# Optimization experiments

Measured on AMD Instinct MI355X. Metric: run time of the kernel, lower is better.

## Reference

```python
import jax, jax.numpy as jnp
import numpy as np

B, S = 128, 1024
IN_NUM, IN_STATE = 64, 16
FEAT = 256
HID = 512
NUM_CLS = 32
EMB_WORD, EMB_DIM = 32, 4
LN_EPS = 1e-5


def _layer_norm(x):
    mu = jnp.mean(x, axis=-1, keepdims=True)
    var = jnp.var(x, axis=-1, keepdims=True)
    return (x - mu) * jax.lax.rsqrt(var + LN_EPS)


def setup_inputs() -> dict:
    key = jax.random.key(0)
    ks = jax.random.split(key, 20)
    w = lambda k, shape: jax.random.normal(k, shape, dtype=jnp.float32) * 0.05
    inp = {
        'x_num': jax.random.normal(ks[0], (B, S, IN_NUM), dtype=jnp.float32),
        'x_state': jax.random.randint(ks[1], (B, S, IN_STATE), 0, EMB_WORD),
        # numeric-branch MLP (2 layers)
        'num_w0': w(ks[2], (FEAT, IN_NUM)), 'num_b0': jnp.zeros((FEAT,), jnp.float32),
        'num_w1': w(ks[3], (FEAT, FEAT)),   'num_b1': jnp.zeros((FEAT,), jnp.float32),
        # state-branch embedding + MLP
        'emb': w(ks[4], (EMB_WORD, EMB_DIM)),
        'st_w0': w(ks[5], (FEAT, IN_STATE * EMB_DIM)), 'st_b0': jnp.zeros((FEAT,), jnp.float32),
        'st_w1': w(ks[6], (FEAT, FEAT)),               'st_b1': jnp.zeros((FEAT,), jnp.float32),
        # LSTM gate weights: input dim = 2*FEAT
        'Wii': w(ks[7], (HID, 2 * FEAT)),  'Whi': w(ks[8], (HID, HID)),
        'Wif': w(ks[9], (HID, 2 * FEAT)),  'Whf': w(ks[10], (HID, HID)),
        'Wig': w(ks[11], (HID, 2 * FEAT)), 'Whg': w(ks[12], (HID, HID)),
        'Wio': w(ks[13], (HID, 2 * FEAT)), 'Who': w(ks[14], (HID, HID)),
        'Bii': jnp.zeros((HID,), jnp.float32), 'Bhi': jnp.zeros((HID,), jnp.float32),
        'Bif': jnp.zeros((HID,), jnp.float32), 'Bhf': jnp.zeros((HID,), jnp.float32),
        'Big': jnp.zeros((HID,), jnp.float32), 'Bhg': jnp.zeros((HID,), jnp.float32),
        'Bio': jnp.zeros((HID,), jnp.float32), 'Bho': jnp.zeros((HID,), jnp.float32),
        'out_w': w(ks[15], (NUM_CLS, HID)), 'out_b': jnp.zeros((NUM_CLS,), jnp.float32),
    }
    return inp


def _forward(x_num, x_state, num_w0, num_b0, num_w1, num_b1, emb,
             st_w0, st_b0, st_w1, st_b1,
             Wii, Whi, Wif, Whf, Wig, Whg, Wio, Who,
             Bii, Bhi, Bif, Bhf, Big, Bhg, Bio, Bho,
             out_w, out_b):
    b, s = x_num.shape[0], x_num.shape[1]
    # numeric branch: Linear -> relu -> LayerNorm (dropout is identity in eval)
    h = _layer_norm(jax.nn.relu(x_num @ num_w0.T + num_b0))
    h = _layer_norm(jax.nn.relu(h @ num_w1.T + num_b1))
    # state branch: embedding lookup, flatten per step, then MLP
    e = emb[x_state].reshape(b, s, -1)                      # [B,S,IN_STATE*EMB_DIM]
    g = _layer_norm(jax.nn.relu(e @ st_w0.T + st_b0))
    g = _layer_norm(jax.nn.relu(g @ st_w1.T + st_b1))
    x = jnp.concatenate([h, g], axis=2)                     # [B,S,2*FEAT]

    hid = Whi.shape[0]
    h0 = jnp.zeros((b, hid), x.dtype)
    c0 = jnp.zeros((b, hid), x.dtype)

    def step(carry, x_t):
        h_t, c_t = carry
        i_t = jax.nn.sigmoid(x_t @ Wii.T + h_t @ Whi.T + Bii + Bhi)
        f_t = jax.nn.sigmoid(x_t @ Wif.T + h_t @ Whf.T + Bif + Bhf)
        g_t = jnp.tanh(x_t @ Wig.T + h_t @ Whg.T + Big + Bhg)
        o_t = jax.nn.sigmoid(x_t @ Wio.T + h_t @ Who.T + Bio + Bho)
        c_new = f_t * c_t + i_t * g_t
        h_new = o_t * jnp.tanh(c_new)
        return (h_new, c_new), None

    (h_last, _), _ = jax.lax.scan(step, (h0, c0), jnp.swapaxes(x, 0, 1))
    return h_last @ out_w.T + out_b                          # [B, num_cls]


def reference(x_num, x_state, num_w0, num_b0, num_w1, num_b1, emb,
              st_w0, st_b0, st_w1, st_b1,
              Wii, Whi, Wif, Whf, Wig, Whg, Wio, Who,
              Bii, Bhi, Bif, Bhf, Big, Bhg, Bio, Bho,
              out_w, out_b):
    return _forward(x_num, x_state, num_w0, num_b0, num_w1, num_b1, emb,
                    st_w0, st_b0, st_w1, st_b1,
                    Wii, Whi, Wif, Whf, Wig, Whg, Wio, Who,
                    Bii, Bhi, Bif, Bhf, Big, Bhg, Bio, Bho,
                    out_w, out_b)
```

## Files before the change

### kernel.cpp

```cpp
#include <hip/hip_runtime.h>
#include <hip/hip_bf16.h>

typedef __attribute__((ext_vector_type(4))) float f4;
typedef __attribute__((ext_vector_type(4))) float f32x4;
typedef __attribute__((ext_vector_type(8))) short bf16x8;
typedef __attribute__((ext_vector_type(4))) unsigned u32x4;
typedef unsigned long long ull;

#define OFF_XCAT   0ull
#define OFF_WCAT   134217728ull
#define OFF_BIAS   138412032ull
#define OFF_HW     138420224ull
#define OFF_CTR    138944512ull
#define WS_NEED    138945536ull

__device__ inline unsigned short f2bf(float x){
  unsigned u = __float_as_uint(x);
  unsigned r = (u + 0x7FFFu + ((u >> 16) & 1u)) >> 16;
  return (unsigned short)r;
}
__device__ inline float bf2f(unsigned short s){ return __uint_as_float(((unsigned)s) << 16); }

__global__ void __launch_bounds__(256) diag_write(float* out, float val){
  out[blockIdx.x * 256 + threadIdx.x] = val;
}

__global__ void __launch_bounds__(256) prep_w(
    const float* Wii, const float* Wif, const float* Wig, const float* Wio,
    const float* Whi, const float* Whf, const float* Whg, const float* Who,
    const float* Bii, const float* Bif, const float* Big, const float* Bio,
    const float* Bhi, const float* Bhf, const float* Bhg, const float* Bho,
    unsigned short* Wcat, float* bias_cat){
  int e = blockIdx.x * 256 + threadIdx.x;
  int col = e >> 10, k = e & 1023;
  int u = col >> 2, g = col & 3;
  float v;
  if (k < 512){
    const float* p = (g==0)?Wii:((g==1)?Wif:((g==2)?Wig:Wio));
    v = p[u*512 + k];
  } else {
    const float* p = (g==0)?Whi:((g==1)?Whf:((g==2)?Whg:Who));
    v = p[u*512 + (k-512)];
  }
  Wcat[e] = f2bf(v);
  if (e < 2048){
    int u2 = e >> 2, g2 = e & 3;
    const float* bx = (g2==0)?Bii:((g2==1)?Bif:((g2==2)?Big:Bio));
    const float* bh = (g2==0)?Bhi:((g2==1)?Bhf:((g2==2)?Bhg:Bho));
    bias_cat[e] = bx[u2] + bh[u2];
  }
}

__global__ void __launch_bounds__(256) stageA_fused(
    const float* __restrict__ xnum, const int* __restrict__ xstate,
    const float* __restrict__ emb,
    const float* __restrict__ num_w0, const float* __restrict__ num_b0,
    const float* __restrict__ num_w1, const float* __restrict__ num_b1,
    const float* __restrict__ st_w0,  const float* __restrict__ st_b0,
    const float* __restrict__ st_w1,  const float* __restrict__ st_b1,
    unsigned short* __restrict__ Xcat){
  __shared__ float Wt[32*256];
  __shared__ float xb[16*68];
  __shared__ float h1[16*260];
  int tid = threadIdx.x;
  long tok0 = (long)blockIdx.x * 16;
  int tg = tid >> 6, c4 = tid & 63;

  #pragma unroll 1
  for (int br = 0; br < 2; ++br){
    const float* W0 = br ? st_w0 : num_w0;
    const float* b0 = br ? st_b0 : num_b0;
    const float* W1 = br ? st_w1 : num_w1;
    const float* b1 = br ? st_b1 : num_b1;

    __syncthreads();
    if (br == 0){
      int tk = tid >> 4, q = tid & 15;
      f4 v = *(const f4*)(xnum + (tok0+tk)*64 + q*4);
      float* d = xb + tk*68 + q*4;
      d[0]=v.x; d[1]=v.y; d[2]=v.z; d[3]=v.w;
    } else {
      int tk = tid >> 4, j = tid & 15;
      int idx = xstate[(tok0+tk)*16 + j];
      f4 v = *(const f4*)(emb + idx*4);
      float* d = xb + tk*68 + j*4;
      d[0]=v.x; d[1]=v.y; d[2]=v.z; d[3]=v.w;
    }

    float acc[4][4];
    { f4 bv = *(const f4*)(b0 + c4*4);
      #pragma unroll
      for (int j=0;j<4;j++){ acc[j][0]=bv.x; acc[j][1]=bv.y; acc[j][2]=bv.z; acc[j][3]=bv.w; } }
    for (int kh=0; kh<2; ++kh){
      __syncthreads();
      { int c = tid;
        const f4* src = (const f4*)(W0 + c*64 + kh*32);
        #pragma unroll
        for (int q=0;q<8;q++){
          f4 v = src[q];
          Wt[(q*4+0)*256 + c] = v.x; Wt[(q*4+1)*256 + c] = v.y;
          Wt[(q*4+2)*256 + c] = v.z; Wt[(q*4+3)*256 + c] = v.w;
        }
      }
      __syncthreads();
      for (int kq=0; kq<8; kq++){
        int k0 = kh*32 + kq*4;
        f4 a0 = *(const f4*)(xb + (tg*4+0)*68 + k0);
        f4 a1 = *(const f4*)(xb + (tg*4+1)*68 + k0);
        f4 a2 = *(const f4*)(xb + (tg*4+2)*68 + k0);
        f4 a3 = *(const f4*)(xb + (tg*4+3)*68 + k0);
        f4 w0 = *(const f4*)(Wt + (kq*4+0)*256 + c4*4);
        f4 w1 = *(const f4*)(Wt + (kq*4+1)*256 + c4*4);
        f4 w2 = *(const f4*)(Wt + (kq*4+2)*256 + c4*4);
        f4 w3 = *(const f4*)(Wt + (kq*4+3)*256 + c4*4);
        #pragma unroll
        for (int j=0;j<4;j++){
          f4 a = (j==0)?a0:((j==1)?a1:((j==2)?a2:a3));
          #pragma unroll
          for (int d=0; d<4; d++)
            acc[j][d] += a.x*w0[d] + a.y*w1[d] + a.z*w2[d] + a.w*w3[d];
        }
      }
    }
    #pragma unroll
    for (int j=0;j<4;j++){
      float v0=fmaxf(acc[j][0],0.f), v1=fmaxf(acc[j][1],0.f);
      float v2=fmaxf(acc[j][2],0.f), v3=fmaxf(acc[j][3],0.f);
      float s1 = v0+v1+v2+v3, s2 = v0*v0+v1*v1+v2*v2+v3*v3;
      for (int off=1; off<64; off<<=1){ s1 += __shfl_xor(s1, off); s2 += __shfl_xor(s2, off); }
      float mu = s1 * (1.f/256.f);
      float rs = rsqrtf(s2*(1.f/256.f) - mu*mu + 1e-5f);
      f4 o; o.x=(v0-mu)*rs; o.y=(v1-mu)*rs; o.z=(v2-mu)*rs; o.w=(v3-mu)*rs;
      *(f4*)(h1 + (tg*4+j)*260 + c4*4) = o;
    }

    float ac2[4][4];
    { f4 bv = *(const f4*)(b1 + c4*4);
      #pragma unroll
      for (int j=0;j<4;j++){ ac2[j][0]=bv.x; ac2[j][1]=bv.y; ac2[j][2]=bv.z; ac2[j][3]=bv.w; } }
    for (int kh=0; kh<8; ++kh){
      __syncthreads();
      { int c = tid;
        const f4* src = (const f4*)(W1 + c*256 + kh*32);
        #pragma unroll
        for (int q=0;q<8;q++){
          f4 v = src[q];
          Wt[(q*4+0)*256 + c] = v.x; Wt[(q*4+1)*256 + c] = v.y;
          Wt[(q*4+2)*256 + c] = v.z; Wt[(q*4+3)*256 + c] = v.w;
        }
      }
      __syncthreads();
      for (int kq=0; kq<8; kq++){
        int k0 = kh*32 + kq*4;
        f4 a0 = *(const f4*)(h1 + (tg*4+0)*260 + k0);
        f4 a1 = *(const f4*)(h1 + (tg*4+1)*260 + k0);
        f4 a2 = *(const f4*)(h1 + (tg*4+2)*260 + k0);
        f4 a3 = *(const f4*)(h1 + (tg*4+3)*260 + k0);
        f4 w0 = *(const f4*)(Wt + (kq*4+0)*256 + c4*4);
        f4 w1 = *(const f4*)(Wt + (kq*4+1)*256 + c4*4);
        f4 w2 = *(const f4*)(Wt + (kq*4+2)*256 + c4*4);
        f4 w3 = *(const f4*)(Wt + (kq*4+3)*256 + c4*4);
        #pragma unroll
        for (int j=0;j<4;j++){
          f4 a = (j==0)?a0:((j==1)?a1:((j==2)?a2:a3));
          #pragma unroll
          for (int d=0; d<4; d++)
            ac2[j][d] += a.x*w0[d] + a.y*w1[d] + a.z*w2[d] + a.w*w3[d];
        }
      }
    }
    #pragma unroll
    for (int j=0;j<4;j++){
      float v0=fmaxf(ac2[j][0],0.f), v1=fmaxf(ac2[j][1],0.f);
      float v2=fmaxf(ac2[j][2],0.f), v3=fmaxf(ac2[j][3],0.f);
      float s1 = v0+v1+v2+v3, s2 = v0*v0+v1*v1+v2*v2+v3*v3;
      for (int off=1; off<64; off<<=1){ s1 += __shfl_xor(s1, off); s2 += __shfl_xor(s2, off); }
      float mu = s1 * (1.f/256.f);
      float rs = rsqrtf(s2*(1.f/256.f) - mu*mu + 1e-5f);
      long tok = tok0 + tg*4 + j;
      long bb = tok >> 10, ss = tok & 1023;
      unsigned short* o = Xcat + (ss*128 + bb)*512 + br*256 + c4*4;
      unsigned lo = (unsigned)f2bf((v0-mu)*rs) | ((unsigned)f2bf((v1-mu)*rs) << 16);
      unsigned hi = (unsigned)f2bf((v2-mu)*rs) | ((unsigned)f2bf((v3-mu)*rs) << 16);
      ((unsigned*)o)[0] = lo; ((unsigned*)o)[1] = hi;
    }
  }
}

__device__ __forceinline__ void ld8x16_sc1(const unsigned* p, u32x4* v){
  asm volatile(
    "global_load_dwordx4 %0, %8, off sc1\n\t"
    "global_load_dwordx4 %1, %8, off offset:256 sc1\n\t"
    "global_load_dwordx4 %2, %8, off offset:512 sc1\n\t"
    "global_load_dwordx4 %3, %8, off offset:768 sc1\n\t"
    "global_load_dwordx4 %4, %8, off offset:1024 sc1\n\t"
    "global_load_dwordx4 %5, %8, off offset:1280 sc1\n\t"
    "global_load_dwordx4 %6, %8, off offset:1536 sc1\n\t"
    "global_load_dwordx4 %7, %8, off offset:1792 sc1\n\t"
    "s_waitcnt vmcnt(0)"
    : "=&v"(v[0]),"=&v"(v[1]),"=&v"(v[2]),"=&v"(v[3]),
      "=&v"(v[4]),"=&v"(v[5]),"=&v"(v[6]),"=&v"(v[7])
    : "v"(p) : "memory");
}

__global__ void __launch_bounds__(256, 1) lstm_pk(
    const unsigned short* __restrict__ Xcat,
    const unsigned short* __restrict__ Wcat,
    const float* __restrict__ bias_cat,
    unsigned int* __restrict__ hw,
    unsigned int* __restrict__ ctr){
  __shared__ __align__(16) char actb[32768];
  __shared__ int okf, sdead;
  int tid = threadIdx.x;
  int lane = tid & 63, w = tid >> 6;
  int g = blockIdx.x & 7, m = blockIdx.x >> 3;

  int colg = 64*m + 16*w + (lane & 15);
  bf16x8 wf[32];
  {
    const bf16x8* wsrc = (const bf16x8*)(Wcat + (long)colg*1024 + (lane>>4)*8);
    #pragma unroll
    for (int s=0;s<32;s++) wf[s] = wsrc[s*4];
  }
  int cb = 64*m + 16*w + 4*(lane>>4);
  f32x4 bias4;
  bias4.x = bias_cat[cb+0]; bias4.y = bias_cat[cb+1];
  bias4.z = bias_cat[cb+2]; bias4.w = bias_cat[cb+3];

  if (tid == 0){
    __hip_atomic_fetch_add(&ctr[255], 1u, __ATOMIC_RELAXED, __HIP_MEMORY_SCOPE_AGENT);
    unsigned v = 0; int it = 0;
    do {
      v = __hip_atomic_load(&ctr[255], __ATOMIC_RELAXED, __HIP_MEMORY_SCOPE_AGENT);
      if (v >= 256u) break;
      __builtin_amdgcn_s_sleep(8);
    } while (++it < 2000000);
    okf = (v >= 256u) ? 1 : 0;
    sdead = 0;
  }
  __syncthreads();
  if (!okf) return;

  float cst = 0.f;
  int r16 = tid >> 4, q16 = tid & 15;

  f32x4 acc0, acc1;
  {
    bf16x8 xf[16];
    const bf16x8* xsrc = (const bf16x8*)(Xcat + ((long)0*128 + g*16 + (lane&15))*512 + (lane>>4)*8);
    #pragma unroll
    for (int s=0;s<16;s++) xf[s] = xsrc[s*4];
    acc0 = bias4;
    acc1.x=0.f; acc1.y=0.f; acc1.z=0.f; acc1.w=0.f;
    #pragma unroll
    for (int s=0;s<16;s+=2){
      acc0 = __builtin_amdgcn_mfma_f32_16x16x32_bf16(wf[s],   xf[s],   acc0, 0, 0, 0);
      acc1 = __builtin_amdgcn_mfma_f32_16x16x32_bf16(wf[s+1], xf[s+1], acc1, 0, 0, 0);
    }
  }

  #pragma unroll 1
  for (int t=0; t<1024; ++t){
    if (t == 0){
      char* hl = actb;
      #pragma unroll
      for (int i=0;i<8;i++){
        int byt = (r16*1024 + q16*8 + i*128) ^ ((r16 & 7) << 4);
        *(ull*)(hl + byt) = 0ull;
      }
    } else {
      const unsigned* hp = hw + ((long)(t&1)*65536) + g*8192 + r16*512 + q16*4;
      u32x4 hv[8];
      unsigned tt = (unsigned)t; int itc = 0;
      for (;;){
        ld8x16_sc1(hp, hv);
        unsigned bad = 0;
        #pragma unroll
        for (int i=0;i<8;i++){
          bad |= (hv[i].x & 0xFFFFu) ^ tt;
          bad |= (hv[i].y & 0xFFFFu) ^ tt;
          bad |= (hv[i].z & 0xFFFFu) ^ tt;
          bad |= (hv[i].w & 0xFFFFu) ^ tt;
        }
        if (!bad) break;
        if ((itc & 31) == 31 && *(volatile int*)&sdead) break;
        if (++itc > 200000){
          *(volatile int*)&sdead = 1;
          __hip_atomic_store(&ctr[252], tt, __ATOMIC_RELAXED, __HIP_MEMORY_SCOPE_AGENT);
          break;
        }
      }
      char* hl = actb + (t&1)*16384;
      #pragma unroll
      for (int i=0;i<8;i++){
        unsigned p0 = (hv[i].x >> 16) | (hv[i].y & 0xFFFF0000u);
        unsigned p1 = (hv[i].z >> 16) | (hv[i].w & 0xFFFF0000u);
        ull pp = (ull)p0 | ((ull)p1 << 32);
        int byt = (r16*1024 + q16*8 + i*128) ^ ((r16 & 7) << 4);
        *(ull*)(hl + byt) = pp;
      }
    }
    __syncthreads();
    if (*(volatile int*)&sdead) break;
    {
      const char* hl = actb + (t&1)*16384;
      #pragma unroll
      for (int s=0;s<16;s+=2){
        int by0 = ((lane&15)*1024 + s*64     + (lane>>4)*16) ^ (((lane&15)&7) << 4);
        int by1 = ((lane&15)*1024 + (s+1)*64 + (lane>>4)*16) ^ (((lane&15)&7) << 4);
        bf16x8 b0 = *(const bf16x8*)(hl + by0);
        bf16x8 b1 = *(const bf16x8*)(hl + by1);
        acc0 = __builtin_amdgcn_mfma_f32_16x16x32_bf16(wf[16+s], b0, acc0, 0, 0, 0);
        acc1 = __builtin_amdgcn_mfma_f32_16x16x32_bf16(wf[17+s], b1, acc1, 0, 0, 0);
      }
    }
    float gi = acc0.x + acc1.x, gf = acc0.y + acc1.y;
    float gg = acc0.z + acc1.z, go = acc0.w + acc1.w;
    float iv = 1.f / (1.f + __expf(-gi));
    float fv = 1.f / (1.f + __expf(-gf));
    float e2 = __expf(-2.f * gg);
    float gv = (1.f - e2) / (1.f + e2);
    float ov = 1.f / (1.f + __expf(-go));
    cst = fv * cst + iv * gv;
    float e2c = __expf(-2.f * cst);
    float hout = ov * (1.f - e2c) / (1.f + e2c);
    {
      unsigned short hb16 = f2bf(hout);
      int unit = 16*m + 4*w + (lane >> 4);
      int row  = lane & 15;
      unsigned word = ((unsigned)hb16 << 16) | (unsigned)(t+1);
      unsigned int* dst = hw + ((long)((t+1)&1)*65536) + g*8192 + row*512 + unit;
      __hip_atomic_store(dst, word, __ATOMIC_RELAXED, __HIP_MEMORY_SCOPE_AGENT);
    }
    {
      int tn = (t < 1023) ? (t+1) : 1023;
      bf16x8 xf[16];
      const bf16x8* xsrc = (const bf16x8*)(Xcat + ((long)tn*128 + g*16 + (lane&15))*512 + (lane>>4)*8);
      #pragma unroll
      for (int s=0;s<16;s++) xf[s] = xsrc[s*4];
      acc0 = bias4;
      acc1.x=0.f; acc1.y=0.f; acc1.z=0.f; acc1.w=0.f;
      #pragma unroll
      for (int s=0;s<16;s+=2){
        acc0 = __builtin_amdgcn_mfma_f32_16x16x32_bf16(wf[s],   xf[s],   acc0, 0, 0, 0);
        acc1 = __builtin_amdgcn_mfma_f32_16x16x32_bf16(wf[s+1], xf[s+1], acc1, 0, 0, 0);
      }
    }
  }

  __syncthreads();
  if (tid == 0 && !sdead)
    __hip_atomic_fetch_add(&ctr[251], 1u, __ATOMIC_RELAXED, __HIP_MEMORY_SCOPE_AGENT);
}

__global__ void __launch_bounds__(256) out_gemm(
    const unsigned int* __restrict__ hw, const unsigned int* __restrict__ ctr,
    const float* __restrict__ out_w, const float* __restrict__ out_b,
    float* __restrict__ out){
  unsigned done = ctr[251], arriv = ctr[255], dead = ctr[252];
  if (dead != 0u || done != 256u){
    float v = dead ? (20000.f + (float)dead) : (10000.f + (float)arriv);
    if (threadIdx.x < 32) out[blockIdx.x*32 + threadIdx.x] = v;
    return;
  }
  __shared__ float part[8][32];
  int b = blockIdx.x;
  int g = b >> 4, r = b & 15;
  const unsigned int* hrow = hw + (long)g*8192 + r*512;
  int col = threadIdx.x & 31, p = threadIdx.x >> 5;
  float s = 0.f;
  for (int u = p*64; u < p*64 + 64; ++u)
    s += bf2f((unsigned short)(hrow[u] >> 16)) * out_w[col*512 + u];
  part[p][col] = s;
  __syncthreads();
  if (p == 0){
    float t = out_b[col];
    #pragma unroll
    for (int i=0;i<8;i++) t += part[i][col];
    out[b*32 + col] = t;
  }
}

extern "C" void kernel_launch(void* const* d_in, const int* in_sizes, int n_in,
                              void* d_out, int out_size, void* d_ws, size_t ws_size,
                              hipStream_t stream){
  const float* x_num   = (const float*)d_in[0];
  const int*   x_state = (const int*)d_in[1];
  const float* num_w0  = (const float*)d_in[2];
  const float* num_b0  = (const float*)d_in[3];
  const float* num_w1  = (const float*)d_in[4];
  const float* num_b1  = (const float*)d_in[5];
  const float* emb     = (const float*)d_in[6];
  const float* st_w0   = (const float*)d_in[7];
  const float* st_b0   = (const float*)d_in[8];
  const float* st_w1   = (const float*)d_in[9];
  const float* st_b1   = (const float*)d_in[10];
  const float* Wii = (const float*)d_in[11];
  const float* Whi = (const float*)d_in[12];
  const float* Wif = (const float*)d_in[13];
  const float* Whf = (const float*)d_in[14];
  const float* Wig = (const float*)d_in[15];
  const float* Whg = (const float*)d_in[16];
  const float* Wio = (const float*)d_in[17];
  const float* Who = (const float*)d_in[18];
  const float* Bii = (const float*)d_in[19];
  const float* Bhi = (const float*)d_in[20];
  const float* Bif = (const float*)d_in[21];
  const float* Bhf = (const float*)d_in[22];
  const float* Big = (const float*)d_in[23];
  const float* Bhg = (const float*)d_in[24];
  const float* Bio = (const float*)d_in[25];
  const float* Bho = (const float*)d_in[26];
  const float* out_w = (const float*)d_in[27];
  const float* out_b = (const float*)d_in[28];

  float* out = (float*)d_out;

  diag_write<<<16, 256, 0, stream>>>(out, 50000.f);

  if (ws_size < WS_NEED){
    diag_write<<<16, 256, 0, stream>>>(out, 100000.f + (float)(ws_size >> 20));
    return;
  }

  char* ws = (char*)d_ws;
  unsigned short* Xcat = (unsigned short*)(ws + OFF_XCAT);
  unsigned short* Wcat = (unsigned short*)(ws + OFF_WCAT);
  float* bias_cat      = (float*)(ws + OFF_BIAS);
  unsigned int* hw     = (unsigned int*)(ws + OFF_HW);
  unsigned int* ctr    = (unsigned int*)(ws + OFF_CTR);

  hipMemsetAsync(ws + OFF_HW, 0, 524288 + 1024, stream);

  prep_w<<<8192, 256, 0, stream>>>(Wii, Wif, Wig, Wio, Whi, Whf, Whg, Who,
                                   Bii, Bif, Big, Bio, Bhi, Bhf, Bhg, Bho,
                                   Wcat, bias_cat);

  stageA_fused<<<8192, 256, 0, stream>>>(x_num, x_state, emb,
                                         num_w0, num_b0, num_w1, num_b1,
                                         st_w0, st_b0, st_w1, st_b1, Xcat);

  lstm_pk<<<256, 256, 0, stream>>>(Xcat, Wcat, bias_cat, hw, ctr);

  out_gemm<<<128, 256, 0, stream>>>(hw, ctr, out_w, out_b, out);
}
```

Before: 5.262 ms.

## Process two batch groups per LSTM block to halve persistent grid size

Each persistent LSTM block now handles two batch groups (gA, gB), interleaving their recurrent phases within each timestep, so the grid shrinks from 256 to 128 blocks. Each block's register-resident weight fragment is reused for both groups, and while one group waits on its h-flags from other blocks the other group can make progress. The second group's h buffer lives in dynamic shared memory, and the arrival and completion counters are adjusted to 128. The cost is more serial work per block and per-step latency, since each block now does two group phases, each with its own barrier.

```diff
diff --git a/kernel.cpp b/kernel.cpp
--- a/kernel.cpp
+++ b/kernel.cpp
@@ -203,17 +203,103 @@
     : "v"(p) : "memory");
 }
 
+#define LSTM_PHASE(GRP, LBASE, CST, ACC0, ACC1)                                          \
+  {                                                                                      \
+    int tn = (t < 1023) ? (t+1) : 1023;                                                  \
+    const bf16x8* xsrc = (const bf16x8*)(Xcat + ((long)tn*128 + (GRP)*16 + (lane&15))*512 + (lane>>4)*8); \
+    bf16x8 xf[16];                                                                       \
+    _Pragma("unroll")                                                                    \
+    for (int s=0;s<16;s++) xf[s] = xsrc[s*4];                                            \
+    if (t == 0){                                                                         \
+      char* hl = (LBASE);                                                                \
+      _Pragma("unroll")                                                                  \
+      for (int i=0;i<8;i++){                                                             \
+        int byt = (r16*1024 + q16*8 + i*128) ^ ((r16 & 7) << 4);                         \
+        *(ull*)(hl + byt) = 0ull;                                                        \
+      }                                                                                  \
+    } else {                                                                             \
+      const unsigned* hp = hw + ((long)(t&1)*65536) + (GRP)*8192 + r16*512 + q16*4;      \
+      u32x4 hv[8];                                                                       \
+      unsigned tt = (unsigned)t; int itc = 0;                                            \
+      for (;;){                                                                          \
+        ld8x16_sc1(hp, hv);                                                              \
+        unsigned bad = 0;                                                                \
+        _Pragma("unroll")                                                                \
+        for (int i=0;i<8;i++){                                                           \
+          bad |= (hv[i].x & 0xFFFFu) ^ tt;  bad |= (hv[i].y & 0xFFFFu) ^ tt;             \
+          bad |= (hv[i].z & 0xFFFFu) ^ tt;  bad |= (hv[i].w & 0xFFFFu) ^ tt;             \
+        }                                                                                \
+        if (!bad) break;                                                                 \
+        if ((itc & 31) == 31 && *(volatile int*)&sdead) break;                           \
+        if (++itc > 200000){                                                             \
+          *(volatile int*)&sdead = 1;                                                    \
+          __hip_atomic_store(&ctr[252], tt, __ATOMIC_RELAXED, __HIP_MEMORY_SCOPE_AGENT); \
+          break;                                                                         \
+        }                                                                                \
+      }                                                                                  \
+      char* hl = (LBASE) + (t&1)*16384;                                                  \
+      _Pragma("unroll")                                                                  \
+      for (int i=0;i<8;i++){                                                             \
+        unsigned p0 = (hv[i].x >> 16) | (hv[i].y & 0xFFFF0000u);                         \
+        unsigned p1 = (hv[i].z >> 16) | (hv[i].w & 0xFFFF0000u);                         \
+        ull pp = (ull)p0 | ((ull)p1 << 32);                                              \
+        int byt = (r16*1024 + q16*8 + i*128) ^ ((r16 & 7) << 4);                         \
+        *(ull*)(hl + byt) = pp;                                                          \
+      }                                                                                  \
+    }                                                                                    \
+    __syncthreads();                                                                     \
+    if (!*(volatile int*)&sdead){                                                        \
+      const char* hl = (LBASE) + (t&1)*16384;                                            \
+      _Pragma("unroll")                                                                  \
+      for (int s=0;s<16;s+=2){                                                           \
+        int by0 = ((lane&15)*1024 + s*64     + (lane>>4)*16) ^ (((lane&15)&7) << 4);     \
+        int by1 = ((lane&15)*1024 + (s+1)*64 + (lane>>4)*16) ^ (((lane&15)&7) << 4);     \
+        bf16x8 b0 = *(const bf16x8*)(hl + by0);                                          \
+        bf16x8 b1 = *(const bf16x8*)(hl + by1);                                          \
+        ACC0 = __builtin_amdgcn_mfma_f32_16x16x32_bf16(wf[16+s], b0, ACC0, 0, 0, 0);     \
+        ACC1 = __builtin_amdgcn_mfma_f32_16x16x32_bf16(wf[17+s], b1, ACC1, 0, 0, 0);     \
+      }                                                                                  \
+      float gi = ACC0.x + ACC1.x, gf = ACC0.y + ACC1.y;                                  \
+      float gg = ACC0.z + ACC1.z, go = ACC0.w + ACC1.w;                                  \
+      float iv = 1.f / (1.f + __expf(-gi));                                              \
+      float fv = 1.f / (1.f + __expf(-gf));                                              \
+      float e2 = __expf(-2.f * gg);                                                      \
+      float gv = (1.f - e2) / (1.f + e2);                                                \
+      float ov = 1.f / (1.f + __expf(-go));                                              \
+      CST = fv * CST + iv * gv;                                                          \
+      float e2c = __expf(-2.f * CST);                                                    \
+      float hout = ov * (1.f - e2c) / (1.f + e2c);                                       \
+      {                                                                                  \
+        unsigned short hb16 = f2bf(hout);                                                \
+        int unit = 16*m + 4*w + (lane >> 4);                                             \
+        int row  = lane & 15;                                                            \
+        unsigned word = ((unsigned)hb16 << 16) | (unsigned)(t+1);                        \
+        unsigned int* dst = hw + ((long)((t+1)&1)*65536) + (GRP)*8192 + row*512 + unit;  \
+        __hip_atomic_store(dst, word, __ATOMIC_RELAXED, __HIP_MEMORY_SCOPE_AGENT);       \
+      }                                                                                  \
+      ACC0 = bias4;                                                                      \
+      ACC1.x=0.f; ACC1.y=0.f; ACC1.z=0.f; ACC1.w=0.f;                                    \
+      _Pragma("unroll")                                                                  \
+      for (int s=0;s<16;s+=2){                                                           \
+        ACC0 = __builtin_amdgcn_mfma_f32_16x16x32_bf16(wf[s],   xf[s],   ACC0, 0, 0, 0); \
+        ACC1 = __builtin_amdgcn_mfma_f32_16x16x32_bf16(wf[s+1], xf[s+1], ACC1, 0, 0, 0); \
+      }                                                                                  \
+    }                                                                                    \
+  }
+
 __global__ void __launch_bounds__(256, 1) lstm_pk(
     const unsigned short* __restrict__ Xcat,
     const unsigned short* __restrict__ Wcat,
     const float* __restrict__ bias_cat,
     unsigned int* __restrict__ hw,
     unsigned int* __restrict__ ctr){
-  __shared__ __align__(16) char actb[32768];
+  __shared__ __align__(16) char actbA[32768];
+  extern __shared__ __align__(16) char actbB[];
   __shared__ int okf, sdead;
   int tid = threadIdx.x;
   int lane = tid & 63, w = tid >> 6;
-  int g = blockIdx.x & 7, m = blockIdx.x >> 3;
+  int pr = blockIdx.x & 3, m = blockIdx.x >> 2;
+  int gA = pr*2, gB = pr*2 + 1;
 
   int colg = 64*m + 16*w + (lane & 15);
   bf16x8 wf[32];
@@ -232,120 +318,47 @@
     unsigned v = 0; int it = 0;
     do {
       v = __hip_atomic_load(&ctr[255], __ATOMIC_RELAXED, __HIP_MEMORY_SCOPE_AGENT);
-      if (v >= 256u) break;
+      if (v >= 128u) break;
       __builtin_amdgcn_s_sleep(8);
     } while (++it < 2000000);
-    okf = (v >= 256u) ? 1 : 0;
+    okf = (v >= 128u) ? 1 : 0;
     sdead = 0;
   }
   __syncthreads();
   if (!okf) return;
 
-  float cst = 0.f;
+  float cstA = 0.f, cstB = 0.f;
   int r16 = tid >> 4, q16 = tid & 15;
 
-  f32x4 acc0, acc1;
+  f32x4 aA0, aA1, aB0, aB1;
   {
     bf16x8 xf[16];
-    const bf16x8* xsrc = (const bf16x8*)(Xcat + ((long)0*128 + g*16 + (lane&15))*512 + (lane>>4)*8);
+    const bf16x8* xsrc = (const bf16x8*)(Xcat + ((long)0*128 + gA*16 + (lane&15))*512 + (lane>>4)*8);
     #pragma unroll
     for (int s=0;s<16;s++) xf[s] = xsrc[s*4];
-    acc0 = bias4;
-    acc1.x=0.f; acc1.y=0.f; acc1.z=0.f; acc1.w=0.f;
+    aA0 = bias4; aA1.x=0.f; aA1.y=0.f; aA1.z=0.f; aA1.w=0.f;
     #pragma unroll
     for (int s=0;s<16;s+=2){
-      acc0 = __builtin_amdgcn_mfma_f32_16x16x32_bf16(wf[s],   xf[s],   acc0, 0, 0, 0);
-      acc1 = __builtin_amdgcn_mfma_f32_16x16x32_bf16(wf[s+1], xf[s+1], acc1, 0, 0, 0);
+      aA0 = __builtin_amdgcn_mfma_f32_16x16x32_bf16(wf[s],   xf[s],   aA0, 0, 0, 0);
+      aA1 = __builtin_amdgcn_mfma_f32_16x16x32_bf16(wf[s+1], xf[s+1], aA1, 0, 0, 0);
+    }
+    const bf16x8* xsrcB = (const bf16x8*)(Xcat + ((long)0*128 + gB*16 + (lane&15))*512 + (lane>>4)*8);
+    #pragma unroll
+    for (int s=0;s<16;s++) xf[s] = xsrcB[s*4];
+    aB0 = bias4; aB1.x=0.f; aB1.y=0.f; aB1.z=0.f; aB1.w=0.f;
+    #pragma unroll
+    for (int s=0;s<16;s+=2){
+      aB0 = __builtin_amdgcn_mfma_f32_16x16x32_bf16(wf[s],   xf[s],   aB0, 0, 0, 0);
+      aB1 = __builtin_amdgcn_mfma_f32_16x16x32_bf16(wf[s+1], xf[s+1], aB1, 0, 0, 0);
     }
   }
 
   #pragma unroll 1
   for (int t=0; t<1024; ++t){
-    if (t == 0){
-      char* hl = actb;
-      #pragma unroll
-      for (int i=0;i<8;i++){
-        int byt = (r16*1024 + q16*8 + i*128) ^ ((r16 & 7) << 4);
-        *(ull*)(hl + byt) = 0ull;
-      }
-    } else {
-      const unsigned* hp = hw + ((long)(t&1)*65536) + g*8192 + r16*512 + q16*4;
-      u32x4 hv[8];
-      unsigned tt = (unsigned)t; int itc = 0;
-      for (;;){
-        ld8x16_sc1(hp, hv);
-        unsigned bad = 0;
-        #pragma unroll
-        for (int i=0;i<8;i++){
-          bad |= (hv[i].x & 0xFFFFu) ^ tt;
-          bad |= (hv[i].y & 0xFFFFu) ^ tt;
-          bad |= (hv[i].z & 0xFFFFu) ^ tt;
-          bad |= (hv[i].w & 0xFFFFu) ^ tt;
-        }
-        if (!bad) break;
-        if ((itc & 31) == 31 && *(volatile int*)&sdead) break;
-        if (++itc > 200000){
-          *(volatile int*)&sdead = 1;
-          __hip_atomic_store(&ctr[252], tt, __ATOMIC_RELAXED, __HIP_MEMORY_SCOPE_AGENT);
-          break;
-        }
-      }
-      char* hl = actb + (t&1)*16384;
-      #pragma unroll
-      for (int i=0;i<8;i++){
-        unsigned p0 = (hv[i].x >> 16) | (hv[i].y & 0xFFFF0000u);
-        unsigned p1 = (hv[i].z >> 16) | (hv[i].w & 0xFFFF0000u);
-        ull pp = (ull)p0 | ((ull)p1 << 32);
-        int byt = (r16*1024 + q16*8 + i*128) ^ ((r16 & 7) << 4);
-        *(ull*)(hl + byt) = pp;
-      }
-    }
-    __syncthreads();
+    LSTM_PHASE(gA, actbA, cstA, aA0, aA1)
     if (*(volatile int*)&sdead) break;
-    {
-      const char* hl = actb + (t&1)*16384;
-      #pragma unroll
-      for (int s=0;s<16;s+=2){
-        int by0 = ((lane&15)*1024 + s*64     + (lane>>4)*16) ^ (((lane&15)&7) << 4);
-        int by1 = ((lane&15)*1024 + (s+1)*64 + (lane>>4)*16) ^ (((lane&15)&7) << 4);
-        bf16x8 b0 = *(const bf16x8*)(hl + by0);
-        bf16x8 b1 = *(const bf16x8*)(hl + by1);
-        acc0 = __builtin_amdgcn_mfma_f32_16x16x32_bf16(wf[16+s], b0, acc0, 0, 0, 0);
-        acc1 = __builtin_amdgcn_mfma_f32_16x16x32_bf16(wf[17+s], b1, acc1, 0, 0, 0);
-      }
-    }
-    float gi = acc0.x + acc1.x, gf = acc0.y + acc1.y;
-    float gg = acc0.z + acc1.z, go = acc0.w + acc1.w;
-    float iv = 1.f / (1.f + __expf(-gi));
-    float fv = 1.f / (1.f + __expf(-gf));
-    float e2 = __expf(-2.f * gg);
-    float gv = (1.f - e2) / (1.f + e2);
-    float ov = 1.f / (1.f + __expf(-go));
-    cst = fv * cst + iv * gv;
-    float e2c = __expf(-2.f * cst);
-    float hout = ov * (1.f - e2c) / (1.f + e2c);
-    {
-      unsigned short hb16 = f2bf(hout);
-      int unit = 16*m + 4*w + (lane >> 4);
-      int row  = lane & 15;
-      unsigned word = ((unsigned)hb16 << 16) | (unsigned)(t+1);
-      unsigned int* dst = hw + ((long)((t+1)&1)*65536) + g*8192 + row*512 + unit;
-      __hip_atomic_store(dst, word, __ATOMIC_RELAXED, __HIP_MEMORY_SCOPE_AGENT);
-    }
-    {
-      int tn = (t < 1023) ? (t+1) : 1023;
-      bf16x8 xf[16];
-      const bf16x8* xsrc = (const bf16x8*)(Xcat + ((long)tn*128 + g*16 + (lane&15))*512 + (lane>>4)*8);
-      #pragma unroll
-      for (int s=0;s<16;s++) xf[s] = xsrc[s*4];
-      acc0 = bias4;
-      acc1.x=0.f; acc1.y=0.f; acc1.z=0.f; acc1.w=0.f;
-      #pragma unroll
-      for (int s=0;s<16;s+=2){
-        acc0 = __builtin_amdgcn_mfma_f32_16x16x32_bf16(wf[s],   xf[s],   acc0, 0, 0, 0);
-        acc1 = __builtin_amdgcn_mfma_f32_16x16x32_bf16(wf[s+1], xf[s+1], acc1, 0, 0, 0);
-      }
-    }
+    LSTM_PHASE(gB, actbB, cstB, aB0, aB1)
+    if (*(volatile int*)&sdead) break;
   }
 
   __syncthreads();
@@ -358,7 +371,7 @@
     const float* __restrict__ out_w, const float* __restrict__ out_b,
     float* __restrict__ out){
   unsigned done = ctr[251], arriv = ctr[255], dead = ctr[252];
-  if (dead != 0u || done != 256u){
+  if (dead != 0u || done != 128u){
     float v = dead ? (20000.f + (float)dead) : (10000.f + (float)arriv);
     if (threadIdx.x < 32) out[blockIdx.x*32 + threadIdx.x] = v;
     return;
@@ -440,7 +453,9 @@
                                          num_w0, num_b0, num_w1, num_b1,
                                          st_w0, st_b0, st_w1, st_b1, Xcat);
 
-  lstm_pk<<<256, 256, 0, stream>>>(Xcat, Wcat, bias_cat, hw, ctr);
+  hipFuncSetAttribute((const void*)lstm_pk,
+                      hipFuncAttributeMaxDynamicSharedMemorySize, 53248);
+  lstm_pk<<<128, 256, 53248, stream>>>(Xcat, Wcat, bias_cat, hw, ctr);
 
   out_gemm<<<128, 256, 0, stream>>>(hw, ctr, out_w, out_b, out);
 }
```

New measurement: 8.736 ms. +66.0%, slower.

## Poll hidden state directly into MFMA operands, removing LDS staging and block barrier

Applied to the files above, without the earlier changes.

Each lane now spin-loads its own 16-byte h slices straight from the global exchange buffer in MFMA B-operand layout. The valid slices are repacked in registers and fed to the MFMA immediately, chunk by chunk. This removes the shared-memory write/read round trip and the per-timestep __syncthreads, letting waves proceed independently and overlap polling with compute. The cost is sixteen smaller serialized poll loops per step, with waits on each, and it relies on the t=0 buffer holding zeros tagged 0.

```diff
diff --git a/kernel.cpp b/kernel.cpp
--- a/kernel.cpp
+++ b/kernel.cpp
@@ -187,29 +187,12 @@
   }
 }
 
-__device__ __forceinline__ void ld8x16_sc1(const unsigned* p, u32x4* v){
-  asm volatile(
-    "global_load_dwordx4 %0, %8, off sc1\n\t"
-    "global_load_dwordx4 %1, %8, off offset:256 sc1\n\t"
-    "global_load_dwordx4 %2, %8, off offset:512 sc1\n\t"
-    "global_load_dwordx4 %3, %8, off offset:768 sc1\n\t"
-    "global_load_dwordx4 %4, %8, off offset:1024 sc1\n\t"
-    "global_load_dwordx4 %5, %8, off offset:1280 sc1\n\t"
-    "global_load_dwordx4 %6, %8, off offset:1536 sc1\n\t"
-    "global_load_dwordx4 %7, %8, off offset:1792 sc1\n\t"
-    "s_waitcnt vmcnt(0)"
-    : "=&v"(v[0]),"=&v"(v[1]),"=&v"(v[2]),"=&v"(v[3]),
-      "=&v"(v[4]),"=&v"(v[5]),"=&v"(v[6]),"=&v"(v[7])
-    : "v"(p) : "memory");
-}
-
 __global__ void __launch_bounds__(256, 1) lstm_pk(
     const unsigned short* __restrict__ Xcat,
     const unsigned short* __restrict__ Wcat,
     const float* __restrict__ bias_cat,
     unsigned int* __restrict__ hw,
     unsigned int* __restrict__ ctr){
-  __shared__ __align__(16) char actb[32768];
   __shared__ int okf, sdead;
   int tid = threadIdx.x;
   int lane = tid & 63, w = tid >> 6;
@@ -242,7 +225,6 @@
   if (!okf) return;
 
   float cst = 0.f;
-  int r16 = tid >> 4, q16 = tid & 15;
 
   f32x4 acc0, acc1;
   {
@@ -259,60 +241,42 @@
     }
   }
 
+  int bad_t = -1;
+
   #pragma unroll 1
   for (int t=0; t<1024; ++t){
-    if (t == 0){
-      char* hl = actb;
-      #pragma unroll
-      for (int i=0;i<8;i++){
-        int byt = (r16*1024 + q16*8 + i*128) ^ ((r16 & 7) << 4);
-        *(ull*)(hl + byt) = 0ull;
-      }
-    } else {
-      const unsigned* hp = hw + ((long)(t&1)*65536) + g*8192 + r16*512 + q16*4;
-      u32x4 hv[8];
-      unsigned tt = (unsigned)t; int itc = 0;
+    unsigned tt = (unsigned)t & 0xFFFFu;
+    const unsigned* hbase = hw + ((long)(t&1)*65536) + g*8192 + (lane&15)*512 + (lane>>4)*8;
+    #pragma unroll 4
+    for (int s=0;s<16;s++){
+      u32x4 v0, v1;
+      int itc = 0;
+      const unsigned* p = hbase + 32*s;
       for (;;){
-        ld8x16_sc1(hp, hv);
-        unsigned bad = 0;
-        #pragma unroll
-        for (int i=0;i<8;i++){
-          bad |= (hv[i].x & 0xFFFFu) ^ tt;
-          bad |= (hv[i].y & 0xFFFFu) ^ tt;
-          bad |= (hv[i].z & 0xFFFFu) ^ tt;
-          bad |= (hv[i].w & 0xFFFFu) ^ tt;
-        }
+        asm volatile(
+          "global_load_dwordx4 %0, %2, off sc1\n\t"
+          "global_load_dwordx4 %1, %2, off offset:16 sc1\n\t"
+          "s_waitcnt vmcnt(0)"
+          : "=&v"(v0), "=&v"(v1) : "v"(p) : "memory");
+        unsigned bad = ((v0.x^tt)|(v0.y^tt)|(v0.z^tt)|(v0.w^tt)
+                       |(v1.x^tt)|(v1.y^tt)|(v1.z^tt)|(v1.w^tt)) & 0xFFFFu;
         if (!bad) break;
-        if ((itc & 31) == 31 && *(volatile int*)&sdead) break;
-        if (++itc > 200000){
-          *(volatile int*)&sdead = 1;
-          __hip_atomic_store(&ctr[252], tt, __ATOMIC_RELAXED, __HIP_MEMORY_SCOPE_AGENT);
-          break;
-        }
-      }
-      char* hl = actb + (t&1)*16384;
-      #pragma unroll
-      for (int i=0;i<8;i++){
-        unsigned p0 = (hv[i].x >> 16) | (hv[i].y & 0xFFFF0000u);
-        unsigned p1 = (hv[i].z >> 16) | (hv[i].w & 0xFFFF0000u);
-        ull pp = (ull)p0 | ((ull)p1 << 32);
-        int byt = (r16*1024 + q16*8 + i*128) ^ ((r16 & 7) << 4);
-        *(ull*)(hl + byt) = pp;
-      }
-    }
-    __syncthreads();
-    if (*(volatile int*)&sdead) break;
-    {
-      const char* hl = actb + (t&1)*16384;
-      #pragma unroll
-      for (int s=0;s<16;s+=2){
-        int by0 = ((lane&15)*1024 + s*64     + (lane>>4)*16) ^ (((lane&15)&7) << 4);
-        int by1 = ((lane&15)*1024 + (s+1)*64 + (lane>>4)*16) ^ (((lane&15)&7) << 4);
-        bf16x8 b0 = *(const bf16x8*)(hl + by0);
-        bf16x8 b1 = *(const bf16x8*)(hl + by1);
-        acc0 = __builtin_amdgcn_mfma_f32_16x16x32_bf16(wf[16+s], b0, acc0, 0, 0, 0);
-        acc1 = __builtin_amdgcn_mfma_f32_16x16x32_bf16(wf[17+s], b1, acc1, 0, 0, 0);
-      }
+        if (++itc > 300000){ bad_t = t; break; }
+        if ((itc & 255) == 255 && *(volatile int*)&sdead) { bad_t = t; break; }
+      }
+      if (bad_t >= 0) break;
+      union { unsigned u[4]; bf16x8 b; } cv;
+      cv.u[0] = (v0.x >> 16) | (v0.y & 0xFFFF0000u);
+      cv.u[1] = (v0.z >> 16) | (v0.w & 0xFFFF0000u);
+      cv.u[2] = (v1.x >> 16) | (v1.y & 0xFFFF0000u);
+      cv.u[3] = (v1.z >> 16) | (v1.w & 0xFFFF0000u);
+      if (s & 1) acc1 = __builtin_amdgcn_mfma_f32_16x16x32_bf16(wf[16+s], cv.b, acc1, 0, 0, 0);
+      else       acc0 = __builtin_amdgcn_mfma_f32_16x16x32_bf16(wf[16+s], cv.b, acc0, 0, 0, 0);
+    }
+    if (bad_t >= 0){
+      *(volatile int*)&sdead = 1;
+      __hip_atomic_store(&ctr[252], (unsigned)(bad_t+1), __ATOMIC_RELAXED, __HIP_MEMORY_SCOPE_AGENT);
+      break;
     }
     float gi = acc0.x + acc1.x, gf = acc0.y + acc1.y;
     float gg = acc0.z + acc1.z, go = acc0.w + acc1.w;
@@ -328,7 +292,7 @@
       unsigned short hb16 = f2bf(hout);
       int unit = 16*m + 4*w + (lane >> 4);
       int row  = lane & 15;
-      unsigned word = ((unsigned)hb16 << 16) | (unsigned)(t+1);
+      unsigned word = ((unsigned)hb16 << 16) | (unsigned)((t+1) & 0xFFFF);
       unsigned int* dst = hw + ((long)((t+1)&1)*65536) + g*8192 + row*512 + unit;
       __hip_atomic_store(dst, word, __ATOMIC_RELAXED, __HIP_MEMORY_SCOPE_AGENT);
     }
```

Result: slower. 14.16 ms (+169.0%).

## Halve persistent LSTM grid so each block computes two gate column groups

Applied to the files above, without the earlier changes.

The persistent LSTM kernel now runs 128 blocks instead of 256. Each wave holds two sets of gate weights in registers and computes two hidden units per lane, issuing twice as many MFMAs and writing two h values per step. The aim is to cut the number of blocks that poll and exchange the hidden state every timestep, reducing cross-block sync and redundant h reads. In exchange, per-block compute per step doubles and register pressure rises sharply, with a risk of spilling.

```diff
diff --git a/kernel.cpp b/kernel.cpp
--- a/kernel.cpp
+++ b/kernel.cpp
@@ -215,47 +215,57 @@
   int lane = tid & 63, w = tid >> 6;
   int g = blockIdx.x & 7, m = blockIdx.x >> 3;
 
-  int colg = 64*m + 16*w + (lane & 15);
-  bf16x8 wf[32];
+  bf16x8 wf[64];
   {
-    const bf16x8* wsrc = (const bf16x8*)(Wcat + (long)colg*1024 + (lane>>4)*8);
-    #pragma unroll
-    for (int s=0;s<32;s++) wf[s] = wsrc[s*4];
-  }
-  int cb = 64*m + 16*w + 4*(lane>>4);
-  f32x4 bias4;
-  bias4.x = bias_cat[cb+0]; bias4.y = bias_cat[cb+1];
-  bias4.z = bias_cat[cb+2]; bias4.w = bias_cat[cb+3];
+    #pragma unroll
+    for (int c=0;c<2;c++){
+      int colg = 128*m + 64*c + 16*w + (lane & 15);
+      const bf16x8* wsrc = (const bf16x8*)(Wcat + (long)colg*1024 + (lane>>4)*8);
+      #pragma unroll
+      for (int s=0;s<32;s++) wf[c*32+s] = wsrc[s*4];
+    }
+  }
+  f32x4 bias4A, bias4B;
+  {
+    int cbA = 128*m + 16*w + 4*(lane>>4);
+    int cbB = cbA + 64;
+    bias4A.x = bias_cat[cbA+0]; bias4A.y = bias_cat[cbA+1];
+    bias4A.z = bias_cat[cbA+2]; bias4A.w = bias_cat[cbA+3];
+    bias4B.x = bias_cat[cbB+0]; bias4B.y = bias_cat[cbB+1];
+    bias4B.z = bias_cat[cbB+2]; bias4B.w = bias_cat[cbB+3];
+  }
 
   if (tid == 0){
     __hip_atomic_fetch_add(&ctr[255], 1u, __ATOMIC_RELAXED, __HIP_MEMORY_SCOPE_AGENT);
     unsigned v = 0; int it = 0;
     do {
       v = __hip_atomic_load(&ctr[255], __ATOMIC_RELAXED, __HIP_MEMORY_SCOPE_AGENT);
-      if (v >= 256u) break;
+      if (v >= 128u) break;
       __builtin_amdgcn_s_sleep(8);
     } while (++it < 2000000);
-    okf = (v >= 256u) ? 1 : 0;
+    okf = (v >= 128u) ? 1 : 0;
     sdead = 0;
   }
   __syncthreads();
   if (!okf) return;
 
-  float cst = 0.f;
+  float cstA = 0.f, cstB = 0.f;
   int r16 = tid >> 4, q16 = tid & 15;
 
-  f32x4 acc0, acc1;
+  f32x4 aA0, aA1, aB0, aB1;
   {
     bf16x8 xf[16];
     const bf16x8* xsrc = (const bf16x8*)(Xcat + ((long)0*128 + g*16 + (lane&15))*512 + (lane>>4)*8);
     #pragma unroll
     for (int s=0;s<16;s++) xf[s] = xsrc[s*4];
-    acc0 = bias4;
-    acc1.x=0.f; acc1.y=0.f; acc1.z=0.f; acc1.w=0.f;
+    aA0 = bias4A; aA1.x=0.f; aA1.y=0.f; aA1.z=0.f; aA1.w=0.f;
+    aB0 = bias4B; aB1.x=0.f; aB1.y=0.f; aB1.z=0.f; aB1.w=0.f;
     #pragma unroll
     for (int s=0;s<16;s+=2){
-      acc0 = __builtin_amdgcn_mfma_f32_16x16x32_bf16(wf[s],   xf[s],   acc0, 0, 0, 0);
-      acc1 = __builtin_amdgcn_mfma_f32_16x16x32_bf16(wf[s+1], xf[s+1], acc1, 0, 0, 0);
+      aA0 = __builtin_amdgcn_mfma_f32_16x16x32_bf16(wf[s],    xf[s],   aA0, 0, 0, 0);
+      aA1 = __builtin_amdgcn_mfma_f32_16x16x32_bf16(wf[s+1],  xf[s+1], aA1, 0, 0, 0);
+      aB0 = __builtin_amdgcn_mfma_f32_16x16x32_bf16(wf[32+s], xf[s],   aB0, 0, 0, 0);
+      aB1 = __builtin_amdgcn_mfma_f32_16x16x32_bf16(wf[33+s], xf[s+1], aB1, 0, 0, 0);
     }
   }
 
@@ -310,27 +320,46 @@
         int by1 = ((lane&15)*1024 + (s+1)*64 + (lane>>4)*16) ^ (((lane&15)&7) << 4);
         bf16x8 b0 = *(const bf16x8*)(hl + by0);
         bf16x8 b1 = *(const bf16x8*)(hl + by1);
-        acc0 = __builtin_amdgcn_mfma_f32_16x16x32_bf16(wf[16+s], b0, acc0, 0, 0, 0);
-        acc1 = __builtin_amdgcn_mfma_f32_16x16x32_bf16(wf[17+s], b1, acc1, 0, 0, 0);
-      }
-    }
-    float gi = acc0.x + acc1.x, gf = acc0.y + acc1.y;
-    float gg = acc0.z + acc1.z, go = acc0.w + acc1.w;
-    float iv = 1.f / (1.f + __expf(-gi));
-    float fv = 1.f / (1.f + __expf(-gf));
-    float e2 = __expf(-2.f * gg);
-    float gv = (1.f - e2) / (1.f + e2);
-    float ov = 1.f / (1.f + __expf(-go));
-    cst = fv * cst + iv * gv;
-    float e2c = __expf(-2.f * cst);
-    float hout = ov * (1.f - e2c) / (1.f + e2c);
+        aA0 = __builtin_amdgcn_mfma_f32_16x16x32_bf16(wf[16+s], b0, aA0, 0, 0, 0);
+        aA1 = __builtin_amdgcn_mfma_f32_16x16x32_bf16(wf[17+s], b1, aA1, 0, 0, 0);
+        aB0 = __builtin_amdgcn_mfma_f32_16x16x32_bf16(wf[48+s], b0, aB0, 0, 0, 0);
+        aB1 = __builtin_amdgcn_mfma_f32_16x16x32_bf16(wf[49+s], b1, aB1, 0, 0, 0);
+      }
+    }
+    unsigned wordA, wordB;
     {
-      unsigned short hb16 = f2bf(hout);
-      int unit = 16*m + 4*w + (lane >> 4);
+      float gi = aA0.x + aA1.x, gf = aA0.y + aA1.y;
+      float gg = aA0.z + aA1.z, go = aA0.w + aA1.w;
+      float iv = 1.f / (1.f + __expf(-gi));
+      float fv = 1.f / (1.f + __expf(-gf));
+      float e2 = __expf(-2.f * gg);
+      float gv = (1.f - e2) / (1.f + e2);
+      float ov = 1.f / (1.f + __expf(-go));
+      cstA = fv * cstA + iv * gv;
+      float e2c = __expf(-2.f * cstA);
+      float hout = ov * (1.f - e2c) / (1.f + e2c);
+      wordA = ((unsigned)f2bf(hout) << 16) | (unsigned)((t+1) & 0xFFFF);
+    }
+    {
+      float gi = aB0.x + aB1.x, gf = aB0.y + aB1.y;
+      float gg = aB0.z + aB1.z, go = aB0.w + aB1.w;
+      float iv = 1.f / (1.f + __expf(-gi));
+      float fv = 1.f / (1.f + __expf(-gf));
+      float e2 = __expf(-2.f * gg);
+      float gv = (1.f - e2) / (1.f + e2);
+      float ov = 1.f / (1.f + __expf(-go));
+      cstB = fv * cstB + iv * gv;
+      float e2c = __expf(-2.f * cstB);
+      float hout = ov * (1.f - e2c) / (1.f + e2c);
+      wordB = ((unsigned)f2bf(hout) << 16) | (unsigned)((t+1) & 0xFFFF);
+    }
+    {
       int row  = lane & 15;
-      unsigned word = ((unsigned)hb16 << 16) | (unsigned)(t+1);
-      unsigned int* dst = hw + ((long)((t+1)&1)*65536) + g*8192 + row*512 + unit;
-      __hip_atomic_store(dst, word, __ATOMIC_RELAXED, __HIP_MEMORY_SCOPE_AGENT);
+      int unitA = 32*m + 4*w + (lane >> 4);
+      int unitB = unitA + 16;
+      unsigned int* base = hw + ((long)((t+1)&1)*65536) + g*8192 + row*512;
+      __hip_atomic_store(base + unitA, wordA, __ATOMIC_RELAXED, __HIP_MEMORY_SCOPE_AGENT);
+      __hip_atomic_store(base + unitB, wordB, __ATOMIC_RELAXED, __HIP_MEMORY_SCOPE_AGENT);
     }
     {
       int tn = (t < 1023) ? (t+1) : 1023;
@@ -338,12 +367,14 @@
       const bf16x8* xsrc = (const bf16x8*)(Xcat + ((long)tn*128 + g*16 + (lane&15))*512 + (lane>>4)*8);
       #pragma unroll
       for (int s=0;s<16;s++) xf[s] = xsrc[s*4];
-      acc0 = bias4;
-      acc1.x=0.f; acc1.y=0.f; acc1.z=0.f; acc1.w=0.f;
+      aA0 = bias4A; aA1.x=0.f; aA1.y=0.f; aA1.z=0.f; aA1.w=0.f;
+      aB0 = bias4B; aB1.x=0.f; aB1.y=0.f; aB1.z=0.f; aB1.w=0.f;
       #pragma unroll
       for (int s=0;s<16;s+=2){
-        acc0 = __builtin_amdgcn_mfma_f32_16x16x32_bf16(wf[s],   xf[s],   acc0, 0, 0, 0);
-        acc1 = __builtin_amdgcn_mfma_f32_16x16x32_bf16(wf[s+1], xf[s+1], acc1, 0, 0, 0);
+        aA0 = __builtin_amdgcn_mfma_f32_16x16x32_bf16(wf[s],    xf[s],   aA0, 0, 0, 0);
+        aA1 = __builtin_amdgcn_mfma_f32_16x16x32_bf16(wf[s+1],  xf[s+1], aA1, 0, 0, 0);
+        aB0 = __builtin_amdgcn_mfma_f32_16x16x32_bf16(wf[32+s], xf[s],   aB0, 0, 0, 0);
+        aB1 = __builtin_amdgcn_mfma_f32_16x16x32_bf16(wf[33+s], xf[s+1], aB1, 0, 0, 0);
       }
     }
   }
@@ -358,7 +389,7 @@
     const float* __restrict__ out_w, const float* __restrict__ out_b,
     float* __restrict__ out){
   unsigned done = ctr[251], arriv = ctr[255], dead = ctr[252];
-  if (dead != 0u || done != 256u){
+  if (dead != 0u || done != 128u){
     float v = dead ? (20000.f + (float)dead) : (10000.f + (float)arriv);
     if (threadIdx.x < 32) out[blockIdx.x*32 + threadIdx.x] = v;
     return;
@@ -440,7 +471,7 @@
                                          num_w0, num_b0, num_w1, num_b1,
                                          st_w0, st_b0, st_w1, st_b1, Xcat);
 
-  lstm_pk<<<256, 256, 0, stream>>>(Xcat, Wcat, bias_cat, hw, ctr);
+  lstm_pk<<<128, 256, 0, stream>>>(Xcat, Wcat, bias_cat, hw, ctr);
 
   out_gemm<<<128, 256, 0, stream>>>(hw, ctr, out_w, out_b, out);
 }
```

Result: slower. 6.920 ms (+31.5%).
